# Kernel optimization log

Measured on AMD Instinct MI355X. Metric: run time of the kernel, lower is better.

## Reference

```python
import jax, jax.numpy as jnp
import numpy as np

B, TQ, TK, D, V = 16, 64, 512, 256, 32000


def setup_inputs() -> dict:
    key = jax.random.key(0)
    k = jax.random.split(key, 8)
    return {
        "domainslots": jax.random.normal(k[0], (B, TQ, D), jnp.float32),
        "out_states": jax.random.normal(k[1], (B, TQ, D), jnp.float32),
        "context": jax.random.normal(k[2], (B, TK, D), jnp.float32),
        "context_plain": jax.random.randint(k[3], (B, TK), 0, V, jnp.int64 if jax.config.jax_enable_x64 else jnp.int32),
        "W_state": jax.random.normal(k[4], (D, V), jnp.float32) * 0.02,
        "b_state": jnp.zeros((V,), jnp.float32),
        "W_gen": jax.random.normal(k[5], (3 * D, 1), jnp.float32) * 0.02,
        "b_gen": jnp.zeros((1,), jnp.float32),
    }


def reference(domainslots, out_states, context, context_plain, W_state, b_state, W_gen, b_gen):
    d = out_states.shape[-1]
    # pointer attention: softmax(Q K^T / sqrt(d)) over context  -> [B, TQ, TK]
    scores = jnp.einsum("bqd,bkd->bqk", out_states, context) / jnp.sqrt(jnp.asarray(d, out_states.dtype))
    pointer_attn = jax.nn.softmax(scores, axis=-1)

    # generation distribution over vocab  -> [B, TQ, V]
    p_state_vocab = jax.nn.softmax(out_states @ W_state + b_state, axis=-1)

    # copy distribution: scatter-add attention mass onto source token ids
    b_idx = jnp.arange(B)[:, None, None]           # [B,1,1]
    q_idx = jnp.arange(TQ)[None, :, None]          # [1,TQ,1]
    v_idx = context_plain[:, None, :]              # [B,1,TK] broadcast over TQ
    p_state_ptr = jnp.zeros((B, TQ, V), p_state_vocab.dtype).at[b_idx, q_idx, v_idx].add(pointer_attn)

    # attention-weighted context vector  -> [B, TQ, D]
    context_vec = jnp.einsum("bqk,bkd->bqd", pointer_attn, context)

    # generation gate  -> [B, TQ, 1]
    p_gen_vec = jnp.concatenate([out_states, context_vec, domainslots], axis=-1)
    p_state_gen = jax.nn.sigmoid(p_gen_vec @ W_gen + b_gen)

    p_state_out = p_state_gen * p_state_vocab + (1.0 - p_state_gen) * p_state_ptr
    return jnp.log(p_state_out)
```

## Files before the change

### kernel.cpp

```cpp
#include <hip/hip_runtime.h>
#include <math.h>

typedef short short8 __attribute__((ext_vector_type(8)));
typedef float f32x4 __attribute__((ext_vector_type(4)));

#define B_ 16
#define TQ_ 64
#define TK_ 512
#define D_ 256
#define V_ 32000
#define M_ (B_ * TQ_)

__device__ __forceinline__ unsigned short f2bf(float x) {
    unsigned int u = __float_as_uint(x);
    unsigned int r = (u + 0x7fffu + ((u >> 16) & 1u)) >> 16;
    return (unsigned short)r;
}

__device__ __forceinline__ void gload_lds16(const void* g, void* l) {
    __builtin_amdgcn_global_load_lds(
        (const __attribute__((address_space(1))) void*)g,
        (__attribute__((address_space(3))) void*)l, 16, 0, 0);
}

__global__ __launch_bounds__(256) void prep_kernel(
    const float* __restrict__ W, unsigned short* __restrict__ Wt,
    const float* __restrict__ ctx, unsigned short* __restrict__ Cb,
    unsigned short* __restrict__ Ct,
    const float* __restrict__ A, unsigned short* __restrict__ Ab,
    const int* __restrict__ cp, int* __restrict__ nexta, int* __restrict__ leader)
{
    __shared__ float tile[64][65];
    __shared__ __align__(16) int c[TK_];
    const int bid = blockIdx.x;
    const int tid = threadIdx.x;

    if (bid < 16) {
        const int b = bid;
        c[tid] = cp[b * TK_ + tid];
        c[tid + 256] = cp[b * TK_ + 256 + tid];
        __syncthreads();
        for (int k = tid; k < TK_; k += 256) {
            const int v = c[k];
            int fm = 1024, nx = 1024;
#pragma unroll 8
            for (int j0 = 0; j0 < TK_; j0 += 4) {
                const int4 q = *(const int4*)&c[j0];
                if (q.x == v) { fm = min(fm, j0);     if (j0     > k) nx = min(nx, j0);     }
                if (q.y == v) { fm = min(fm, j0 + 1); if (j0 + 1 > k) nx = min(nx, j0 + 1); }
                if (q.z == v) { fm = min(fm, j0 + 2); if (j0 + 2 > k) nx = min(nx, j0 + 2); }
                if (q.w == v) { fm = min(fm, j0 + 3); if (j0 + 3 > k) nx = min(nx, j0 + 3); }
            }
            nexta[b * TK_ + k] = (nx < 1024) ? nx : -1;
            leader[b * TK_ + k] = (fm == k) ? 1 : 0;
        }
    } else if (bid < 2016) {
        const int wb = bid - 16;
        const int k0 = (wb & 3) * 64;
        const int n0 = (wb >> 2) * 64;
#pragma unroll
        for (int i = 0; i < 16; i++) {
            const int r = i * 4 + (tid >> 6), cc = tid & 63;
            tile[r][cc] = W[(k0 + r) * V_ + n0 + cc];
        }
        __syncthreads();
#pragma unroll
        for (int i = 0; i < 4; i++) {
            const int nl = i * 16 + (tid >> 4);
            const int kq = (tid & 15) * 4;
            ushort4 o;
            o.x = f2bf(tile[kq + 0][nl]);
            o.y = f2bf(tile[kq + 1][nl]);
            o.z = f2bf(tile[kq + 2][nl]);
            o.w = f2bf(tile[kq + 3][nl]);
            *(ushort4*)&Wt[(n0 + nl) * D_ + k0 + kq] = o;
        }
    } else if (bid < 2528) {
        const int cbid = bid - 2016;
        const int b = cbid >> 5;
        const int r5 = cbid & 31;
        const int k0 = (r5 >> 2) * 64;
        const int d0 = (r5 & 3) * 64;
#pragma unroll
        for (int i = 0; i < 16; i++) {
            const int r = i * 4 + (tid >> 6), cc = tid & 63;
            const float v = ctx[((b * TK_) + k0 + r) * D_ + d0 + cc];
            tile[r][cc] = v;
            Cb[((b * TK_) + k0 + r) * D_ + d0 + cc] = f2bf(v);
        }
        __syncthreads();
#pragma unroll
        for (int i = 0; i < 4; i++) {
            const int dl = i * 16 + (tid >> 4);
            const int kq = (tid & 15) * 4;
            ushort4 o;
            o.x = f2bf(tile[kq + 0][dl]);
            o.y = f2bf(tile[kq + 1][dl]);
            o.z = f2bf(tile[kq + 2][dl]);
            o.w = f2bf(tile[kq + 3][dl]);
            *(ushort4*)&Ct[((b * D_) + d0 + dl) * TK_ + k0 + kq] = o;
        }
    } else {
        const int i = ((bid - 2528) * 256 + tid) * 4;
        const float4 v = *(const float4*)&A[i];
        ushort4 o;
        o.x = f2bf(v.x); o.y = f2bf(v.y); o.z = f2bf(v.z); o.w = f2bf(v.w);
        *(ushort4*)&Ab[i] = o;
    }
}

template <int LDA, int LDB, int KTOT>
__global__ __launch_bounds__(256) void gemm_small(
    const unsigned short* __restrict__ A,
    const unsigned short* __restrict__ Bt,
    float* __restrict__ C, int ldc, int nchunks, int btrows, float scale)
{
    __shared__ short Al[64][72];
    __shared__ short Bl[128][72];
    const int tid = threadIdx.x;
    const int b = blockIdx.x / nchunks;
    const int n0 = (blockIdx.x % nchunks) * 128;
    A += (size_t)b * 64 * LDA;
    Bt += (size_t)b * btrows * LDB;
    C += (size_t)b * 64 * ldc;

    const int wid = tid >> 6;
    const int lane = tid & 63;
    const int wm = wid & 1, wn = wid >> 1;
    const int quad = lane >> 4, l15 = lane & 15;

    f32x4 acc[2][4];
#pragma unroll
    for (int i = 0; i < 2; i++)
#pragma unroll
        for (int j = 0; j < 4; j++) acc[i][j] = f32x4{0.f, 0.f, 0.f, 0.f};

    for (int k0 = 0; k0 < KTOT; k0 += 64) {
        __syncthreads();
#pragma unroll
        for (int i = 0; i < 2; i++) {
            const int c = tid + i * 256;
            const int r = c >> 3, kc = (c & 7) * 8;
            *(uint4*)&Al[r][kc] = *(const uint4*)&A[r * LDA + k0 + kc];
        }
#pragma unroll
        for (int i = 0; i < 4; i++) {
            const int c = tid + i * 256;
            const int r = c >> 3, kc = (c & 7) * 8;
            *(uint4*)&Bl[r][kc] = *(const uint4*)&Bt[(n0 + r) * LDB + k0 + kc];
        }
        __syncthreads();
#pragma unroll
        for (int ks = 0; ks < 64; ks += 32) {
            short8 af[2], bf[4];
#pragma unroll
            for (int mt = 0; mt < 2; mt++)
                af[mt] = *(const short8*)&Al[wm * 32 + mt * 16 + l15][ks + quad * 8];
#pragma unroll
            for (int nt = 0; nt < 4; nt++)
                bf[nt] = *(const short8*)&Bl[wn * 64 + nt * 16 + l15][ks + quad * 8];
#pragma unroll
            for (int mt = 0; mt < 2; mt++)
#pragma unroll
                for (int nt = 0; nt < 4; nt++)
                    acc[mt][nt] = __builtin_amdgcn_mfma_f32_16x16x32_bf16(
                        af[mt], bf[nt], acc[mt][nt], 0, 0, 0);
        }
    }
#pragma unroll
    for (int mt = 0; mt < 2; mt++)
#pragma unroll
        for (int nt = 0; nt < 4; nt++)
#pragma unroll
            for (int r = 0; r < 4; r++) {
                const int rl = wm * 32 + mt * 16 + quad * 4 + r;
                const int col = n0 + wn * 64 + nt * 16 + l15;
                C[rl * ldc + col] = acc[mt][nt][r] * scale;
            }
}

__global__ __launch_bounds__(256) void softmax_kernel(
    float* __restrict__ S, unsigned short* __restrict__ Pb)
{
    const int w = threadIdx.x >> 6, lane = threadIdx.x & 63;
    const int row = blockIdx.x * 4 + w;
    float v[8], m = -1e30f;
#pragma unroll
    for (int j = 0; j < 8; j++) { v[j] = S[row * TK_ + lane + 64 * j]; m = fmaxf(m, v[j]); }
#pragma unroll
    for (int off = 32; off; off >>= 1) m = fmaxf(m, __shfl_xor(m, off));
    float s = 0.f;
#pragma unroll
    for (int j = 0; j < 8; j++) { v[j] = __expf(v[j] - m); s += v[j]; }
#pragma unroll
    for (int off = 32; off; off >>= 1) s += __shfl_xor(s, off);
    const float inv = 1.0f / s;
#pragma unroll
    for (int j = 0; j < 8; j++) {
        const float p = v[j] * inv;
        S[row * TK_ + lane + 64 * j] = p;
        Pb[row * TK_ + lane + 64 * j] = f2bf(p);
    }
}

__global__ __launch_bounds__(256) void pgen_kernel(
    const float* __restrict__ os, const float* __restrict__ cv,
    const float* __restrict__ dm, const float* __restrict__ W_gen,
    const float* __restrict__ b_gen, float* __restrict__ pg)
{
    const int w = threadIdx.x >> 6, lane = threadIdx.x & 63;
    const int row = blockIdx.x * 4 + w;
    const int d4 = lane * 4;
    const float4 o4 = *(const float4*)&os[row * D_ + d4];
    const float4 c4 = *(const float4*)&cv[row * D_ + d4];
    const float4 m4 = *(const float4*)&dm[row * D_ + d4];
    const float4 w0 = *(const float4*)&W_gen[d4];
    const float4 w1 = *(const float4*)&W_gen[D_ + d4];
    const float4 w2 = *(const float4*)&W_gen[2 * D_ + d4];
    float p = o4.x * w0.x + o4.y * w0.y + o4.z * w0.z + o4.w * w0.w
            + c4.x * w1.x + c4.y * w1.y + c4.z * w1.z + c4.w * w1.w
            + m4.x * w2.x + m4.y * w2.y + m4.z * w2.z + m4.w * w2.w;
#pragma unroll
    for (int off = 32; off; off >>= 1) p += __shfl_xor(p, off);
    if (lane == 0) pg[row] = 1.0f / (1.0f + __expf(-(p + b_gen[0])));
}

__global__ __launch_bounds__(256) void gemm_vocab_z(
    const unsigned short* __restrict__ A,
    const unsigned short* __restrict__ Bt,
    const float* __restrict__ b_state,
    float* __restrict__ Z)
{
    __shared__ short Al[128][64];
    __shared__ short Bl[128][64];
    __shared__ float bst[128];

    const int tid = threadIdx.x;
    const int swz = (blockIdx.x & 7) * 250 + (blockIdx.x >> 3);
    const int m0 = (swz & 7) * 128;
    const int n0 = (swz >> 3) * 128;

    if (tid < 128) bst[tid] = b_state[n0 + tid];

    const int wid = tid >> 6, lane = tid & 63;
    const int wm = wid & 1, wn = wid >> 1;
    const int quad = lane >> 4, l15 = lane & 15;
    const int srow = lane >> 3;
    const int scolz = ((lane & 7) ^ srow) << 3;

    f32x4 acc[4][4];
#pragma unroll
    for (int i = 0; i < 4; i++)
#pragma unroll
        for (int j = 0; j < 4; j++) acc[i][j] = f32x4{0.f, 0.f, 0.f, 0.f};

    for (int k0 = 0; k0 < D_; k0 += 64) {
        __syncthreads();
#pragma unroll
        for (int j = 0; j < 4; j++) {
            const int c = j * 4 + wid;
            const int r = c * 8 + srow;
            gload_lds16(&A[(size_t)(m0 + r) * D_ + k0 + scolz], &Al[c * 8][0]);
        }
#pragma unroll
        for (int j = 0; j < 4; j++) {
            const int c = j * 4 + wid;
            const int r = c * 8 + srow;
            gload_lds16(&Bt[(size_t)(n0 + r) * D_ + k0 + scolz], &Bl[c * 8][0]);
        }
        __syncthreads();
#pragma unroll
        for (int ks = 0; ks < 64; ks += 32) {
            short8 af[4], bf[4];
#pragma unroll
            for (int mt = 0; mt < 4; mt++) {
                const int row = wm * 64 + mt * 16 + l15;
                af[mt] = *(const short8*)&Al[row][(ks + quad * 8) ^ ((l15 & 7) << 3)];
            }
#pragma unroll
            for (int nt = 0; nt < 4; nt++) {
                const int row = wn * 64 + nt * 16 + l15;
                bf[nt] = *(const short8*)&Bl[row][(ks + quad * 8) ^ ((l15 & 7) << 3)];
            }
#pragma unroll
            for (int mt = 0; mt < 4; mt++)
#pragma unroll
                for (int nt = 0; nt < 4; nt++)
                    acc[mt][nt] = __builtin_amdgcn_mfma_f32_16x16x32_bf16(
                        af[mt], bf[nt], acc[mt][nt], 0, 0, 0);
        }
    }

#pragma unroll
    for (int mt = 0; mt < 4; mt++) {
        float rs[4] = {0.f, 0.f, 0.f, 0.f};
#pragma unroll
        for (int nt = 0; nt < 4; nt++) {
            const float bcol = bst[wn * 64 + nt * 16 + l15];
#pragma unroll
            for (int r = 0; r < 4; r++)
                rs[r] += __expf(acc[mt][nt][r] + bcol);
        }
#pragma unroll
        for (int r = 0; r < 4; r++) {
            float v = rs[r];
            v += __shfl_xor(v, 1);
            v += __shfl_xor(v, 2);
            v += __shfl_xor(v, 4);
            v += __shfl_xor(v, 8);
            if (l15 == 0)
                atomicAdd(&Z[m0 + wm * 64 + mt * 16 + quad * 4 + r], v);
        }
    }
}

__global__ __launch_bounds__(256) void gemm_vocab_out(
    const unsigned short* __restrict__ A,
    const unsigned short* __restrict__ Bt,
    const float* __restrict__ b_state,
    const float* __restrict__ pg,
    const float* __restrict__ Z,
    float* __restrict__ out)
{
    __shared__ short Al[128][64];
    __shared__ short Bl[128][64];
    __shared__ float bst[128];
    __shared__ float rcs[128];

    const int tid = threadIdx.x;
    const int swz = (blockIdx.x & 7) * 250 + (blockIdx.x >> 3);
    const int m0 = (swz & 7) * 128;
    const int n0 = (swz >> 3) * 128;

    if (tid < 128) {
        bst[tid] = b_state[n0 + tid];
        rcs[tid] = logf(pg[m0 + tid]) - logf(Z[m0 + tid]);
    }

    const int wid = tid >> 6, lane = tid & 63;
    const int wm = wid & 1, wn = wid >> 1;
    const int quad = lane >> 4, l15 = lane & 15;
    const int srow = lane >> 3;
    const int scolz = ((lane & 7) ^ srow) << 3;

    f32x4 acc[4][4];
#pragma unroll
    for (int i = 0; i < 4; i++)
#pragma unroll
        for (int j = 0; j < 4; j++) acc[i][j] = f32x4{0.f, 0.f, 0.f, 0.f};

    for (int k0 = 0; k0 < D_; k0 += 64) {
        __syncthreads();
#pragma unroll
        for (int j = 0; j < 4; j++) {
            const int c = j * 4 + wid;
            const int r = c * 8 + srow;
            gload_lds16(&A[(size_t)(m0 + r) * D_ + k0 + scolz], &Al[c * 8][0]);
        }
#pragma unroll
        for (int j = 0; j < 4; j++) {
            const int c = j * 4 + wid;
            const int r = c * 8 + srow;
            gload_lds16(&Bt[(size_t)(n0 + r) * D_ + k0 + scolz], &Bl[c * 8][0]);
        }
        __syncthreads();
#pragma unroll
        for (int ks = 0; ks < 64; ks += 32) {
            short8 af[4], bf[4];
#pragma unroll
            for (int mt = 0; mt < 4; mt++) {
                const int row = wm * 64 + mt * 16 + l15;
                af[mt] = *(const short8*)&Al[row][(ks + quad * 8) ^ ((l15 & 7) << 3)];
            }
#pragma unroll
            for (int nt = 0; nt < 4; nt++) {
                const int row = wn * 64 + nt * 16 + l15;
                bf[nt] = *(const short8*)&Bl[row][(ks + quad * 8) ^ ((l15 & 7) << 3)];
            }
#pragma unroll
            for (int mt = 0; mt < 4; mt++)
#pragma unroll
                for (int nt = 0; nt < 4; nt++)
                    acc[mt][nt] = __builtin_amdgcn_mfma_f32_16x16x32_bf16(
                        af[mt], bf[nt], acc[mt][nt], 0, 0, 0);
        }
    }

#pragma unroll
    for (int mt = 0; mt < 4; mt++) {
#pragma unroll
        for (int nt = 0; nt < 4; nt++) {
            const float bcol = bst[wn * 64 + nt * 16 + l15];
#pragma unroll
            for (int r = 0; r < 4; r++) {
                const int row = wm * 64 + mt * 16 + quad * 4 + r;
                const int col = wn * 64 + nt * 16 + l15;
                out[(size_t)(m0 + row) * V_ + n0 + col] = acc[mt][nt][r] + bcol + rcs[row];
            }
        }
    }
}

__global__ __launch_bounds__(256) void fixup_kernel(
    const int* __restrict__ cp, const int* __restrict__ nexta,
    const int* __restrict__ leader, const float* __restrict__ attn,
    const float* __restrict__ pg, float* __restrict__ out)
{
    const int t = blockIdx.x * 256 + threadIdx.x;
    const int row = t >> 9, k = t & 511;
    const int b = row >> 6;
    if (!leader[b * TK_ + k]) return;
    float a = attn[row * TK_ + k];
    int j = nexta[b * TK_ + k];
    while (j >= 0) { a += attn[row * TK_ + j]; j = nexta[b * TK_ + j]; }
    const float val = (1.0f - pg[row]) * a;
    const int v = cp[b * TK_ + k];
    const size_t idx = (size_t)row * V_ + v;
    out[idx] = logf(expf(out[idx]) + val);
}

extern "C" void kernel_launch(void* const* d_in, const int* in_sizes, int n_in,
                              void* d_out, int out_size, void* d_ws, size_t ws_size,
                              hipStream_t stream)
{
    const float* domainslots = (const float*)d_in[0];
    const float* out_states  = (const float*)d_in[1];
    const float* context     = (const float*)d_in[2];
    const int*   cp          = (const int*)d_in[3];
    const float* W_state     = (const float*)d_in[4];
    const float* b_state     = (const float*)d_in[5];
    const float* W_gen       = (const float*)d_in[6];
    const float* b_gen       = (const float*)d_in[7];
    float* out = (float*)d_out;
    char* ws = (char*)d_ws;

    float* Z      = (float*)(ws);
    float* pg     = (float*)(ws + 4096);
    float* S      = (float*)(ws + 12288);
    int* nexta    = (int*)(ws + 2109440);
    int* leader   = (int*)(ws + 2142208);
    unsigned short* Ab = (unsigned short*)(ws + 2174976);
    unsigned short* Wt = (unsigned short*)(ws + 2699264);
    unsigned short* Cb = (unsigned short*)(ws + 19083264);
    unsigned short* Ct = (unsigned short*)(ws + 23277568);
    unsigned short* Pb = (unsigned short*)(ws + 27471872);
    float* cv     = (float*)(ws + 28520448);

    hipMemsetAsync(Z, 0, M_ * sizeof(float), stream);

    prep_kernel<<<2784, 256, 0, stream>>>(W_state, Wt, context, Cb, Ct,
                                          out_states, Ab, cp, nexta, leader);

    gemm_small<D_, D_, D_><<<B_ * 4, 256, 0, stream>>>(Ab, Cb, S, TK_, 4, TK_, 0.0625f);
    softmax_kernel<<<M_ / 4, 256, 0, stream>>>(S, Pb);
    gemm_small<TK_, TK_, TK_><<<B_ * 2, 256, 0, stream>>>(Pb, Ct, cv, D_, 2, D_, 1.0f);
    pgen_kernel<<<M_ / 4, 256, 0, stream>>>(out_states, cv, domainslots, W_gen, b_gen, pg);

    gemm_vocab_z<<<(M_ / 128) * (V_ / 128), 256, 0, stream>>>(Ab, Wt, b_state, Z);
    gemm_vocab_out<<<(M_ / 128) * (V_ / 128), 256, 0, stream>>>(Ab, Wt, b_state, pg, Z, out);
    fixup_kernel<<<(M_ * TK_) / 256, 256, 0, stream>>>(cp, nexta, leader, S, pg, out);
}
```

Baseline: 309.7 us.

## Split vocab Z-pass GEMM across softmax and PV kernels to fill idle CUs

The vocab log-sum-exp pass (gemm_vocab_z) is split into two halves of 1000 blocks each. One half is co-launched with the pointer-softmax blocks and the other with the tiny P·V GEMM blocks, so those small, low-occupancy stages share the GPU with heavy GEMM work instead of running alone. The hipMemsetAsync of Z is folded into an extra block of prep_kernel. The cost is a larger static LDS footprint for the small-stage blocks, plus reliance on block scheduling order for load balance.

```diff
diff --git a/kernel.cpp b/kernel.cpp
--- a/kernel.cpp
+++ b/kernel.cpp
@@ -28,7 +28,8 @@
     const float* __restrict__ ctx, unsigned short* __restrict__ Cb,
     unsigned short* __restrict__ Ct,
     const float* __restrict__ A, unsigned short* __restrict__ Ab,
-    const int* __restrict__ cp, int* __restrict__ nexta, int* __restrict__ leader)
+    const int* __restrict__ cp, int* __restrict__ nexta, int* __restrict__ leader,
+    float* __restrict__ Z)
 {
     __shared__ float tile[64][65];
     __shared__ __align__(16) int c[TK_];
@@ -100,12 +101,14 @@
             o.w = f2bf(tile[kq + 3][dl]);
             *(ushort4*)&Ct[((b * D_) + d0 + dl) * TK_ + k0 + kq] = o;
         }
-    } else {
+    } else if (bid < 2784) {
         const int i = ((bid - 2528) * 256 + tid) * 4;
         const float4 v = *(const float4*)&A[i];
         ushort4 o;
         o.x = f2bf(v.x); o.y = f2bf(v.y); o.z = f2bf(v.z); o.w = f2bf(v.w);
         *(ushort4*)&Ab[i] = o;
+    } else {
+        ((float4*)Z)[tid] = float4{0.f, 0.f, 0.f, 0.f};
     }
 }
 
@@ -179,11 +182,173 @@
             }
 }
 
-__global__ __launch_bounds__(256) void softmax_kernel(
+__device__ __forceinline__ void z_body(
+    int g, const unsigned short* __restrict__ A, const unsigned short* __restrict__ Bt,
+    const float* __restrict__ b_state, float* __restrict__ Z, char* smem)
+{
+    short (*Al)[64] = (short(*)[64])smem;
+    short (*Bl)[64] = (short(*)[64])(smem + 16384);
+    float* bst = (float*)(smem + 32768);
+
+    const int tid = threadIdx.x;
+    const int swz = (g & 7) * 250 + (g >> 3);
+    const int m0 = (swz & 7) * 128;
+    const int n0 = (swz >> 3) * 128;
+
+    if (tid < 128) bst[tid] = b_state[n0 + tid];
+
+    const int wid = tid >> 6, lane = tid & 63;
+    const int wm = wid & 1, wn = wid >> 1;
+    const int quad = lane >> 4, l15 = lane & 15;
+    const int srow = lane >> 3;
+    const int scolz = ((lane & 7) ^ srow) << 3;
+
+    f32x4 acc[4][4];
+#pragma unroll
+    for (int i = 0; i < 4; i++)
+#pragma unroll
+        for (int j = 0; j < 4; j++) acc[i][j] = f32x4{0.f, 0.f, 0.f, 0.f};
+
+    for (int k0 = 0; k0 < D_; k0 += 64) {
+        __syncthreads();
+#pragma unroll
+        for (int j = 0; j < 4; j++) {
+            const int c = j * 4 + wid;
+            const int r = c * 8 + srow;
+            gload_lds16(&A[(size_t)(m0 + r) * D_ + k0 + scolz], &Al[c * 8][0]);
+        }
+#pragma unroll
+        for (int j = 0; j < 4; j++) {
+            const int c = j * 4 + wid;
+            const int r = c * 8 + srow;
+            gload_lds16(&Bt[(size_t)(n0 + r) * D_ + k0 + scolz], &Bl[c * 8][0]);
+        }
+        __syncthreads();
+#pragma unroll
+        for (int ks = 0; ks < 64; ks += 32) {
+            short8 af[4], bf[4];
+#pragma unroll
+            for (int mt = 0; mt < 4; mt++) {
+                const int row = wm * 64 + mt * 16 + l15;
+                af[mt] = *(const short8*)&Al[row][(ks + quad * 8) ^ ((l15 & 7) << 3)];
+            }
+#pragma unroll
+            for (int nt = 0; nt < 4; nt++) {
+                const int row = wn * 64 + nt * 16 + l15;
+                bf[nt] = *(const short8*)&Bl[row][(ks + quad * 8) ^ ((l15 & 7) << 3)];
+            }
+#pragma unroll
+            for (int mt = 0; mt < 4; mt++)
+#pragma unroll
+                for (int nt = 0; nt < 4; nt++)
+                    acc[mt][nt] = __builtin_amdgcn_mfma_f32_16x16x32_bf16(
+                        af[mt], bf[nt], acc[mt][nt], 0, 0, 0);
+        }
+    }
+
+#pragma unroll
+    for (int mt = 0; mt < 4; mt++) {
+        float rs[4] = {0.f, 0.f, 0.f, 0.f};
+#pragma unroll
+        for (int nt = 0; nt < 4; nt++) {
+            const float bcol = bst[wn * 64 + nt * 16 + l15];
+#pragma unroll
+            for (int r = 0; r < 4; r++)
+                rs[r] += __expf(acc[mt][nt][r] + bcol);
+        }
+#pragma unroll
+        for (int r = 0; r < 4; r++) {
+            float v = rs[r];
+            v += __shfl_xor(v, 1);
+            v += __shfl_xor(v, 2);
+            v += __shfl_xor(v, 4);
+            v += __shfl_xor(v, 8);
+            if (l15 == 0)
+                atomicAdd(&Z[m0 + wm * 64 + mt * 16 + quad * 4 + r], v);
+        }
+    }
+}
+
+__device__ __forceinline__ void pv_body(
+    int pvb, const unsigned short* __restrict__ A, const unsigned short* __restrict__ Bt,
+    float* __restrict__ C, char* smem)
+{
+    short (*Al)[72] = (short(*)[72])smem;
+    short (*Bl)[72] = (short(*)[72])(smem + 64 * 72 * 2);
+    const int tid = threadIdx.x;
+    const int b = pvb >> 1;
+    const int n0 = (pvb & 1) * 128;
+    A += (size_t)b * 64 * TK_;
+    Bt += (size_t)b * 256 * TK_;
+    C += (size_t)b * 64 * D_;
+
+    const int wid = tid >> 6;
+    const int lane = tid & 63;
+    const int wm = wid & 1, wn = wid >> 1;
+    const int quad = lane >> 4, l15 = lane & 15;
+
+    f32x4 acc[2][4];
+#pragma unroll
+    for (int i = 0; i < 2; i++)
+#pragma unroll
+        for (int j = 0; j < 4; j++) acc[i][j] = f32x4{0.f, 0.f, 0.f, 0.f};
+
+    for (int k0 = 0; k0 < TK_; k0 += 64) {
+        __syncthreads();
+#pragma unroll
+        for (int i = 0; i < 2; i++) {
+            const int c = tid + i * 256;
+            const int r = c >> 3, kc = (c & 7) * 8;
+            *(uint4*)&Al[r][kc] = *(const uint4*)&A[r * TK_ + k0 + kc];
+        }
+#pragma unroll
+        for (int i = 0; i < 4; i++) {
+            const int c = tid + i * 256;
+            const int r = c >> 3, kc = (c & 7) * 8;
+            *(uint4*)&Bl[r][kc] = *(const uint4*)&Bt[(n0 + r) * TK_ + k0 + kc];
+        }
+        __syncthreads();
+#pragma unroll
+        for (int ks = 0; ks < 64; ks += 32) {
+            short8 af[2], bf[4];
+#pragma unroll
+            for (int mt = 0; mt < 2; mt++)
+                af[mt] = *(const short8*)&Al[wm * 32 + mt * 16 + l15][ks + quad * 8];
+#pragma unroll
+            for (int nt = 0; nt < 4; nt++)
+                bf[nt] = *(const short8*)&Bl[wn * 64 + nt * 16 + l15][ks + quad * 8];
+#pragma unroll
+            for (int mt = 0; mt < 2; mt++)
+#pragma unroll
+                for (int nt = 0; nt < 4; nt++)
+                    acc[mt][nt] = __builtin_amdgcn_mfma_f32_16x16x32_bf16(
+                        af[mt], bf[nt], acc[mt][nt], 0, 0, 0);
+        }
+    }
+#pragma unroll
+    for (int mt = 0; mt < 2; mt++)
+#pragma unroll
+        for (int nt = 0; nt < 4; nt++)
+#pragma unroll
+            for (int r = 0; r < 4; r++) {
+                const int rl = wm * 32 + mt * 16 + quad * 4 + r;
+                const int col = n0 + wn * 64 + nt * 16 + l15;
+                C[rl * D_ + col] = acc[mt][nt][r];
+            }
+}
+
+__global__ __launch_bounds__(256) void zs_kernel(
+    const unsigned short* __restrict__ A, const unsigned short* __restrict__ Wt,
+    const float* __restrict__ b_state, float* __restrict__ Z,
     float* __restrict__ S, unsigned short* __restrict__ Pb)
 {
+    __shared__ __align__(16) char smem[33280];
+    const int bid = blockIdx.x;
+    if (bid < 1000) { z_body(bid, A, Wt, b_state, Z, smem); return; }
+
+    const int sbid = bid - 1000;
     const int w = threadIdx.x >> 6, lane = threadIdx.x & 63;
-    const int row = blockIdx.x * 4 + w;
+    const int row = sbid * 4 + w;
     float v[8], m = -1e30f;
 #pragma unroll
     for (int j = 0; j < 8; j++) { v[j] = S[row * TK_ + lane + 64 * j]; m = fmaxf(m, v[j]); }
@@ -201,6 +366,18 @@
         S[row * TK_ + lane + 64 * j] = p;
         Pb[row * TK_ + lane + 64 * j] = f2bf(p);
     }
+}
+
+__global__ __launch_bounds__(256) void zpv_kernel(
+    const unsigned short* __restrict__ A, const unsigned short* __restrict__ Wt,
+    const float* __restrict__ b_state, float* __restrict__ Z,
+    const unsigned short* __restrict__ Pb, const unsigned short* __restrict__ Ct,
+    float* __restrict__ cv)
+{
+    __shared__ __align__(16) char smem[33280];
+    const int bid = blockIdx.x;
+    if (bid < 1000) { z_body(1000 + bid, A, Wt, b_state, Z, smem); return; }
+    pv_body(bid - 1000, Pb, Ct, cv, smem);
 }
 
 __global__ __launch_bounds__(256) void pgen_kernel(
@@ -225,95 +402,6 @@
     if (lane == 0) pg[row] = 1.0f / (1.0f + __expf(-(p + b_gen[0])));
 }
 
-__global__ __launch_bounds__(256) void gemm_vocab_z(
-    const unsigned short* __restrict__ A,
-    const unsigned short* __restrict__ Bt,
-    const float* __restrict__ b_state,
-    float* __restrict__ Z)
-{
-    __shared__ short Al[128][64];
-    __shared__ short Bl[128][64];
-    __shared__ float bst[128];
-
-    const int tid = threadIdx.x;
-    const int swz = (blockIdx.x & 7) * 250 + (blockIdx.x >> 3);
-    const int m0 = (swz & 7) * 128;
-    const int n0 = (swz >> 3) * 128;
-
-    if (tid < 128) bst[tid] = b_state[n0 + tid];
-
-    const int wid = tid >> 6, lane = tid & 63;
-    const int wm = wid & 1, wn = wid >> 1;
-    const int quad = lane >> 4, l15 = lane & 15;
-    const int srow = lane >> 3;
-    const int scolz = ((lane & 7) ^ srow) << 3;
-
-    f32x4 acc[4][4];
-#pragma unroll
-    for (int i = 0; i < 4; i++)
-#pragma unroll
-        for (int j = 0; j < 4; j++) acc[i][j] = f32x4{0.f, 0.f, 0.f, 0.f};
-
-    for (int k0 = 0; k0 < D_; k0 += 64) {
-        __syncthreads();
-#pragma unroll
-        for (int j = 0; j < 4; j++) {
-            const int c = j * 4 + wid;
-            const int r = c * 8 + srow;
-            gload_lds16(&A[(size_t)(m0 + r) * D_ + k0 + scolz], &Al[c * 8][0]);
-        }
-#pragma unroll
-        for (int j = 0; j < 4; j++) {
-            const int c = j * 4 + wid;
-            const int r = c * 8 + srow;
-            gload_lds16(&Bt[(size_t)(n0 + r) * D_ + k0 + scolz], &Bl[c * 8][0]);
-        }
-        __syncthreads();
-#pragma unroll
-        for (int ks = 0; ks < 64; ks += 32) {
-            short8 af[4], bf[4];
-#pragma unroll
-            for (int mt = 0; mt < 4; mt++) {
-                const int row = wm * 64 + mt * 16 + l15;
-                af[mt] = *(const short8*)&Al[row][(ks + quad * 8) ^ ((l15 & 7) << 3)];
-            }
-#pragma unroll
-            for (int nt = 0; nt < 4; nt++) {
-                const int row = wn * 64 + nt * 16 + l15;
-                bf[nt] = *(const short8*)&Bl[row][(ks + quad * 8) ^ ((l15 & 7) << 3)];
-            }
-#pragma unroll
-            for (int mt = 0; mt < 4; mt++)
-#pragma unroll
-                for (int nt = 0; nt < 4; nt++)
-                    acc[mt][nt] = __builtin_amdgcn_mfma_f32_16x16x32_bf16(
-                        af[mt], bf[nt], acc[mt][nt], 0, 0, 0);
-        }
-    }
-
-#pragma unroll
-    for (int mt = 0; mt < 4; mt++) {
-        float rs[4] = {0.f, 0.f, 0.f, 0.f};
-#pragma unroll
-        for (int nt = 0; nt < 4; nt++) {
-            const float bcol = bst[wn * 64 + nt * 16 + l15];
-#pragma unroll
-            for (int r = 0; r < 4; r++)
-                rs[r] += __expf(acc[mt][nt][r] + bcol);
-        }
-#pragma unroll
-        for (int r = 0; r < 4; r++) {
-            float v = rs[r];
-            v += __shfl_xor(v, 1);
-            v += __shfl_xor(v, 2);
-            v += __shfl_xor(v, 4);
-            v += __shfl_xor(v, 8);
-            if (l15 == 0)
-                atomicAdd(&Z[m0 + wm * 64 + mt * 16 + quad * 4 + r], v);
-        }
-    }
-}
-
 __global__ __launch_bounds__(256) void gemm_vocab_out(
     const unsigned short* __restrict__ A,
     const unsigned short* __restrict__ Bt,
@@ -446,17 +534,18 @@
     unsigned short* Pb = (unsigned short*)(ws + 27471872);
     float* cv     = (float*)(ws + 28520448);
 
-    hipMemsetAsync(Z, 0, M_ * sizeof(float), stream);
-
-    prep_kernel<<<2784, 256, 0, stream>>>(W_state, Wt, context, Cb, Ct,
-                                          out_states, Ab, cp, nexta, leader);
+    prep_kernel<<<2785, 256, 0, stream>>>(W_state, Wt, context, Cb, Ct,
+                                          out_states, Ab, cp, nexta, leader, Z);
 
     gemm_small<D_, D_, D_><<<B_ * 4, 256, 0, stream>>>(Ab, Cb, S, TK_, 4, TK_, 0.0625f);
-    softmax_kernel<<<M_ / 4, 256, 0, stream>>>(S, Pb);
-    gemm_small<TK_, TK_, TK_><<<B_ * 2, 256, 0, stream>>>(Pb, Ct, cv, D_, 2, D_, 1.0f);
+
+    zs_kernel<<<1256, 256, 0, stream>>>(Ab, Wt, b_state, Z, S, Pb);
+
+    zpv_kernel<<<1032, 256, 0, stream>>>(Ab, Wt, b_state, Z, Pb, Ct, cv);
+
     pgen_kernel<<<M_ / 4, 256, 0, stream>>>(out_states, cv, domainslots, W_gen, b_gen, pg);
 
-    gemm_vocab_z<<<(M_ / 128) * (V_ / 128), 256, 0, stream>>>(Ab, Wt, b_state, Z);
     gemm_vocab_out<<<(M_ / 128) * (V_ / 128), 256, 0, stream>>>(Ab, Wt, b_state, pg, Z, out);
+
     fixup_kernel<<<(M_ * TK_) / 256, 256, 0, stream>>>(cp, nexta, leader, S, pg, out);
 }
```

Result: no change. 313.2 us (+1.1%).

## Fuse copy-distribution fixup into vocab GEMM epilogue and fold Z memset into prep

Applied to the files above, without the earlier changes.

Removes the separate fixup kernel. Each vocab GEMM output tile now scans the leader/token lists for its two batches and collects the context tokens whose vocab id falls inside its 128-column window into a shared list. The owning lanes then add the pointer-attention mass directly in the epilogue, overwriting their own earlier store. The Z zeroing is moved from a hipMemsetAsync into an extra block of the prep kernel, cutting two launches. In exchange, every GEMM block pays an extra scan of 1024 leader entries plus shared atomics, and entries beyond 256 matches per tile would be silently dropped.

```diff
diff --git a/kernel.cpp b/kernel.cpp
--- a/kernel.cpp
+++ b/kernel.cpp
@@ -28,7 +28,8 @@
     const float* __restrict__ ctx, unsigned short* __restrict__ Cb,
     unsigned short* __restrict__ Ct,
     const float* __restrict__ A, unsigned short* __restrict__ Ab,
-    const int* __restrict__ cp, int* __restrict__ nexta, int* __restrict__ leader)
+    const int* __restrict__ cp, int* __restrict__ nexta, int* __restrict__ leader,
+    float* __restrict__ Z)
 {
     __shared__ float tile[64][65];
     __shared__ __align__(16) int c[TK_];
@@ -100,12 +101,14 @@
             o.w = f2bf(tile[kq + 3][dl]);
             *(ushort4*)&Ct[((b * D_) + d0 + dl) * TK_ + k0 + kq] = o;
         }
-    } else {
+    } else if (bid < 2784) {
         const int i = ((bid - 2528) * 256 + tid) * 4;
         const float4 v = *(const float4*)&A[i];
         ushort4 o;
         o.x = f2bf(v.x); o.y = f2bf(v.y); o.z = f2bf(v.z); o.w = f2bf(v.w);
         *(ushort4*)&Ab[i] = o;
+    } else {
+        ((float4*)Z)[tid] = float4{0.f, 0.f, 0.f, 0.f};
     }
 }
 
@@ -320,12 +323,18 @@
     const float* __restrict__ b_state,
     const float* __restrict__ pg,
     const float* __restrict__ Z,
+    const int* __restrict__ cp,
+    const int* __restrict__ nexta,
+    const int* __restrict__ leader,
+    const float* __restrict__ S,
     float* __restrict__ out)
 {
     __shared__ short Al[128][64];
     __shared__ short Bl[128][64];
     __shared__ float bst[128];
     __shared__ float rcs[128];
+    __shared__ int mlist[256];
+    __shared__ int nm_sh;
 
     const int tid = threadIdx.x;
     const int swz = (blockIdx.x & 7) * 250 + (blockIdx.x >> 3);
@@ -335,6 +344,21 @@
     if (tid < 128) {
         bst[tid] = b_state[n0 + tid];
         rcs[tid] = logf(pg[m0 + tid]) - logf(Z[m0 + tid]);
+    }
+    if (tid == 0) nm_sh = 0;
+    __syncthreads();
+#pragma unroll
+    for (int h = 0; h < 2; h++) {
+        const int b = (m0 >> 6) + h;
+        for (int k = tid; k < TK_; k += 256) {
+            if (leader[b * TK_ + k]) {
+                const int v = cp[b * TK_ + k];
+                if (v >= n0 && v < n0 + 128) {
+                    const int e = atomicAdd(&nm_sh, 1);
+                    if (e < 256) mlist[e] = (h << 16) | (k << 7) | (v - n0);
+                }
+            }
+        }
     }
 
     const int wid = tid >> 6, lane = tid & 63;
@@ -399,24 +423,31 @@
             }
         }
     }
-}
-
-__global__ __launch_bounds__(256) void fixup_kernel(
-    const int* __restrict__ cp, const int* __restrict__ nexta,
-    const int* __restrict__ leader, const float* __restrict__ attn,
-    const float* __restrict__ pg, float* __restrict__ out)
-{
-    const int t = blockIdx.x * 256 + threadIdx.x;
-    const int row = t >> 9, k = t & 511;
-    const int b = row >> 6;
-    if (!leader[b * TK_ + k]) return;
-    float a = attn[row * TK_ + k];
-    int j = nexta[b * TK_ + k];
-    while (j >= 0) { a += attn[row * TK_ + j]; j = nexta[b * TK_ + j]; }
-    const float val = (1.0f - pg[row]) * a;
-    const int v = cp[b * TK_ + k];
-    const size_t idx = (size_t)row * V_ + v;
-    out[idx] = logf(expf(out[idx]) + val);
+
+    const int nm = (nm_sh < 256) ? nm_sh : 256;
+    for (int e = 0; e < nm; e++) {
+        const int pk = mlist[e];
+        const int cl = pk & 127;
+        const int h  = (pk >> 16) & 1;
+        if ((cl >> 6) == wn && (cl & 15) == l15 && h == wm) {
+            const int nt = (cl >> 4) & 3;
+            const int k  = (pk >> 7) & 511;
+            const int b  = (m0 >> 6) + h;
+#pragma unroll
+            for (int mt = 0; mt < 4; mt++)
+#pragma unroll
+                for (int r = 0; r < 4; r++) {
+                    const int row = wm * 64 + mt * 16 + quad * 4 + r;
+                    const int rr = m0 + row;
+                    float a = S[(size_t)rr * TK_ + k];
+                    int j = nexta[b * TK_ + k];
+                    while (j >= 0) { a += S[(size_t)rr * TK_ + j]; j = nexta[b * TK_ + j]; }
+                    const float v0 = acc[mt][nt][r] + bst[cl] + rcs[row];
+                    out[(size_t)rr * V_ + n0 + cl] =
+                        logf(expf(v0) + (1.0f - pg[rr]) * a);
+                }
+        }
+    }
 }
 
 extern "C" void kernel_launch(void* const* d_in, const int* in_sizes, int n_in,
@@ -446,17 +477,19 @@
     unsigned short* Pb = (unsigned short*)(ws + 27471872);
     float* cv     = (float*)(ws + 28520448);
 
-    hipMemsetAsync(Z, 0, M_ * sizeof(float), stream);
-
-    prep_kernel<<<2784, 256, 0, stream>>>(W_state, Wt, context, Cb, Ct,
-                                          out_states, Ab, cp, nexta, leader);
+    prep_kernel<<<2785, 256, 0, stream>>>(W_state, Wt, context, Cb, Ct,
+                                          out_states, Ab, cp, nexta, leader, Z);
 
     gemm_small<D_, D_, D_><<<B_ * 4, 256, 0, stream>>>(Ab, Cb, S, TK_, 4, TK_, 0.0625f);
+
     softmax_kernel<<<M_ / 4, 256, 0, stream>>>(S, Pb);
+
     gemm_small<TK_, TK_, TK_><<<B_ * 2, 256, 0, stream>>>(Pb, Ct, cv, D_, 2, D_, 1.0f);
+
     pgen_kernel<<<M_ / 4, 256, 0, stream>>>(out_states, cv, domainslots, W_gen, b_gen, pg);
 
     gemm_vocab_z<<<(M_ / 128) * (V_ / 128), 256, 0, stream>>>(Ab, Wt, b_state, Z);
-    gemm_vocab_out<<<(M_ / 128) * (V_ / 128), 256, 0, stream>>>(Ab, Wt, b_state, pg, Z, out);
-    fixup_kernel<<<(M_ * TK_) / 256, 256, 0, stream>>>(cp, nexta, leader, S, pg, out);
-}
+
+    gemm_vocab_out<<<(M_ / 128) * (V_ / 128), 256, 0, stream>>>(
+        Ab, Wt, b_state, pg, Z, cp, nexta, leader, S, out);
+}
```

Result: slower. 416.1 us (+34.4%).
